# Optimization experiments

Hardware: AMD Instinct MI355X
Metric: run time of the kernel (lower is better)

The kernel has to match this reference:

```python
import jax, jax.numpy as jnp
import numpy as np

V, T, H, N, D, L = 32000, 2048, 4, 4096, 256, 6
K = N // H  # head dim = 1024
EPS = 1e-5


def ln(x):
    # LayerNorm over last dim, no affine (elementwise_affine=False)
    mu = jnp.mean(x, axis=-1, keepdims=True)
    var = jnp.mean(jnp.square(x - mu), axis=-1, keepdims=True)
    return (x - mu) / jnp.sqrt(var + EPS)


def rotate_half(x):
    hd = x.shape[-1]
    return jnp.concatenate([-x[..., hd // 2:], x[..., :hd // 2]], axis=-1)


def rope_tables(seq_len, head_dim):
    inv_freq = 1.0 / (10000.0 ** (jnp.arange(0, head_dim, 2, dtype=jnp.float32) / head_dim))
    t = jnp.arange(seq_len, dtype=jnp.float32)
    freqs = t[:, None] * inv_freq[None, :]          # [T, hd/2]
    emb = jnp.concatenate([freqs, freqs], axis=-1)  # [T, hd]
    return jnp.cos(emb), jnp.sin(emb)


def setup_inputs() -> dict:
    key = jax.random.key(0)
    ks = jax.random.split(key, 7)
    input_ = jax.random.randint(ks[0], (2, T), 0, V, dtype=jnp.int32)
    emb = jax.random.normal(ks[1], (V, D), dtype=jnp.float32) * 0.02
    pos = jax.random.normal(ks[2], (T, D), dtype=jnp.float32) * (1.0 / np.sqrt(L))
    Dx = jax.random.normal(ks[3], (H, D, K), dtype=jnp.float32) * 0.02
    Dy = jax.random.normal(ks[4], (H, D, K), dtype=jnp.float32) * 0.02
    E = jax.random.normal(ks[5], (N, D), dtype=jnp.float32) * 0.02
    readout = jax.random.normal(ks[6], (D, V), dtype=jnp.float32) * 0.02
    return {"input_": input_, "emb": emb, "pos": pos, "Dx": Dx, "Dy": Dy, "E": E, "readout": readout}


def reference(input_, emb, pos, Dx, Dy, E, readout):
    B, Tl = input_.shape
    cos, sin = rope_tables(Tl, K)
    cos = cos[None, None]  # [1,1,T,K]
    sin = sin[None, None]
    v = ln(emb[input_])  # [B,T,D]
    for _ in range(L):
        v = v + pos[None]  # abs pos added every layer
        x = jax.nn.relu(jnp.einsum('btd,hdk->bhtk', v, Dx))  # [B,H,T,K]
        q = x * cos + rotate_half(x) * sin                   # RoPE (Q==K)
        scores = jnp.einsum('bhtk,bhsk->bhts', q, q)         # unnormalized, no softmax
        a = jnp.einsum('bhts,bsd->bhtd', scores, v)          # [B,H,T,D]
        y = jax.nn.relu(jnp.einsum('bhtd,hdk->bhtk', ln(a), Dy)) * x  # gated
        y = y.transpose(0, 2, 1, 3).reshape(B, Tl, H * K)    # [B,T,N]
        v = ln(v + ln(y @ E))
    return v @ readout  # [B,T,V]
```

## Files before the change

kernel.cpp:

```cpp
#include <hip/hip_runtime.h>
#include <hip/hip_bf16.h>

using u16 = unsigned short;

#define BB 2
#define TT 2048
#define DD 256
#define HH_ 4
#define KK 1024
#define NN 4096
#define VV 32000
#define BT 4096
#define LL 6

typedef __attribute__((ext_vector_type(8))) short short8;
typedef __attribute__((ext_vector_type(4))) float f32x4;

__device__ __forceinline__ float b2f(u16 u) {
    union { unsigned int i; float f; } cv; cv.i = ((unsigned int)u) << 16; return cv.f;
}
__device__ __forceinline__ u16 f2b(float f) {
    union { float f; unsigned int i; } cv; cv.f = f;
    const unsigned int u = cv.i;
    return (u16)((u + 0x7fffu + ((u >> 16) & 1u)) >> 16);
}
__device__ __forceinline__ float rdF(const float* p) { return *p; }
__device__ __forceinline__ float rdF(const u16* p)   { return b2f(*p); }
__device__ __forceinline__ void stF(float* p, float v) { *p = v; }
__device__ __forceinline__ void stF(u16* p, float v)   { *p = f2b(v); }

__device__ __forceinline__ float block_sum_256(float val, float* sbuf) {
#pragma unroll
    for (int off = 32; off > 0; off >>= 1)
        val += __shfl_down(val, off, 64);
    const int lane = threadIdx.x & 63;
    const int wid  = threadIdx.x >> 6;
    __syncthreads();
    if (lane == 0) sbuf[wid] = val;
    __syncthreads();
    return sbuf[0] + sbuf[1] + sbuf[2] + sbuf[3];
}

__global__ void k_sincos(float* __restrict__ cosH, float* __restrict__ sinH) {
    const int t = blockIdx.x;
    for (int f = threadIdx.x; f < 512; f += blockDim.x) {
        const double invf = exp(-((double)(2 * f) / (double)KK) * 9.210340371976184);
        const double th = (double)t * invf;
        double s, c;
        sincos(th, &s, &c);
        cosH[t * 512 + f] = (float)c;
        sinH[t * 512 + f] = (float)s;
    }
}

__global__ void k_embed_ln(const int* __restrict__ idx, const float* __restrict__ emb,
                           const float* __restrict__ pos,
                           float* __restrict__ v, u16* __restrict__ vbf) {
    __shared__ float sbuf[4];
    const int r = blockIdx.x;
    const int t = r & (TT - 1);
    const int token = idx[r];
    const float xv = emb[(long)token * DD + threadIdx.x];
    const float mu = block_sum_256(xv, sbuf) * (1.f / DD);
    const float d = xv - mu;
    const float var = block_sum_256(d * d, sbuf) * (1.f / DD);
    const float res = d / sqrtf(var + 1e-5f) + pos[t * DD + threadIdx.x];
    v[(long)r * DD + threadIdx.x] = res;
    vbf[(long)r * DD + threadIdx.x] = f2b(res);
}

__global__ void k_ln_rows_out(const float* __restrict__ a, u16* __restrict__ o) {
    __shared__ float sbuf[4];
    const long r = blockIdx.x;
    const float xv = a[r * DD + threadIdx.x];
    const float mu = block_sum_256(xv, sbuf) * (1.f / DD);
    const float d = xv - mu;
    const float var = block_sum_256(d * d, sbuf) * (1.f / DD);
    o[r * DD + threadIdx.x] = f2b(d / sqrtf(var + 1e-5f));
}

__global__ void k_fin_ln(float* __restrict__ v, const float* __restrict__ zp,
                         const float* __restrict__ pos, u16* __restrict__ vbf,
                         int addp) {
    __shared__ float sbuf[4];
    const long r = blockIdx.x;
    const int t = (int)(r & (TT - 1));
    const long i = r * DD + threadIdx.x;
    const long S = (long)BT * DD;
    const float zv = zp[i] + zp[i + S] + zp[i + 2 * S] + zp[i + 3 * S];
    const float mu1 = block_sum_256(zv, sbuf) * (1.f / DD);
    const float d1 = zv - mu1;
    const float var1 = block_sum_256(d1 * d1, sbuf) * (1.f / DD);
    const float lnz = d1 / sqrtf(var1 + 1e-5f);
    const float u = v[i] + lnz;
    const float mu2 = block_sum_256(u, sbuf) * (1.f / DD);
    const float d2 = u - mu2;
    const float var2 = block_sum_256(d2 * d2, sbuf) * (1.f / DD);
    float res = d2 / sqrtf(var2 + 1e-5f);
    if (addp) res += pos[t * DD + threadIdx.x];
    v[i] = res;
    vbf[i] = f2b(res);
}

template <typename TIN>
__global__ __launch_bounds__(256)
void k_trans(const TIN* __restrict__ in, u16* __restrict__ out, int R, int C) {
    __shared__ float tile[32][33];
    const long zo = (long)blockIdx.z * (long)R * (long)C;
    const int r0 = blockIdx.y * 32, c0 = blockIdx.x * 32;
    const int tx = threadIdx.x & 31, ty = threadIdx.x >> 5;
#pragma unroll
    for (int u = 0; u < 32; u += 8)
        tile[ty + u][tx] = rdF(&in[zo + (long)(r0 + ty + u) * C + c0 + tx]);
    __syncthreads();
#pragma unroll
    for (int u = 0; u < 32; u += 8)
        out[zo + (long)(c0 + ty + u) * R + r0 + tx] = f2b(tile[tx][ty + u]);
}

__global__ __launch_bounds__(256)
void k_rope_t(const u16* __restrict__ x, const float* __restrict__ cosH,
              const float* __restrict__ sinH, u16* __restrict__ q, u16* __restrict__ qT) {
    __shared__ u16 Sa[64][72];
    __shared__ u16 Sb[64][72];
    const long zoff = (long)blockIdx.z * TT * KK;
    const int t0 = blockIdx.y * 64;
    const int klo = blockIdx.x * 64;
    const int khi = klo + 512;
    const int tx = threadIdx.x & 63;
    const int ty = threadIdx.x >> 6;
#pragma unroll
    for (int u = 0; u < 64; u += 4) {
        const int t = t0 + u + ty;
        const long rb = (long)t * KK;
        const float xa = b2f(x[zoff + rb + klo + tx]);
        const float xb = b2f(x[zoff + rb + khi + tx]);
        const float ca = cosH[t * 512 + klo + tx];
        const float sa = sinH[t * 512 + klo + tx];
        const float qa = xa * ca - xb * sa;
        const float qb = xb * ca + xa * sa;
        const u16 qab = f2b(qa), qbb = f2b(qb);
        q[zoff + rb + klo + tx] = qab;
        q[zoff + rb + khi + tx] = qbb;
        Sa[u + ty][tx] = qab;
        Sb[u + ty][tx] = qbb;
    }
    __syncthreads();
#pragma unroll
    for (int u = 0; u < 64; u += 4) {
        const int r = u + ty;
        qT[zoff + (long)(klo + r) * TT + t0 + tx] = Sa[tx][r];
        qT[zoff + (long)(khi + r) * TT + t0 + tx] = Sb[tx][r];
    }
}

template <int EPI, typename TC>
__global__ __launch_bounds__(256)
void gemm_mfma(const u16* __restrict__ Ab, const u16* __restrict__ Btb,
               TC* __restrict__ Cb, const u16* __restrict__ Gb,
               int M, int N, int Kin, int lda, int ldb, int ldc, int ldg,
               long sAo, long sAi, long sBo, long sBi,
               long sCo, long sCi, long sGo, long sGi, int HH)
{
    const int z = blockIdx.z;
    const int zo = z / HH, zi = z - zo * HH;
    const u16* A  = Ab  + zo * sAo + zi * sAi;
    const u16* Bt = Btb + zo * sBo + zi * sBi;
    TC* C = Cb + zo * sCo + zi * sCi;
    const u16* G = (EPI == 2) ? (Gb + zo * sGo + zi * sGi) : nullptr;

    const int m0 = blockIdx.y * 128;
    const int n0 = blockIdx.x * 128;
    const int tid = threadIdx.x;
    const int lane = tid & 63;
    const int wv = tid >> 6;
    const int wr = (wv >> 1) * 64;
    const int wc = (wv & 1) * 64;

    __shared__ u16 As[128 * 64];
    __shared__ u16 Bs[128 * 64];

    f32x4 acc[4][4];
    const f32x4 vzero = {0.f, 0.f, 0.f, 0.f};
#pragma unroll
    for (int i = 0; i < 4; ++i)
#pragma unroll
        for (int j = 0; j < 4; ++j) acc[i][j] = vzero;

    const int rbase = tid >> 3;
    const int slot  = tid & 7;
    const u16* Abase = A  + (long)(m0 + rbase) * lda + slot * 8;
    const u16* Bbase = Bt + (long)(n0 + rbase) * ldb + slot * 8;
    const int ldsU = (tid & 192) * 8;

    const int rl = lane & 15;
    const int kg = lane >> 4;

    for (int k0 = 0; k0 < Kin; k0 += 64) {
#pragma unroll
        for (int it = 0; it < 4; ++it) {
            __builtin_amdgcn_global_load_lds(
                (const __attribute__((address_space(1))) unsigned int*)(Abase + (long)it * 32 * lda + k0),
                (__attribute__((address_space(3))) unsigned int*)(As + it * 2048 + ldsU),
                16, 0, 0);
            __builtin_amdgcn_global_load_lds(
                (const __attribute__((address_space(1))) unsigned int*)(Bbase + (long)it * 32 * ldb + k0),
                (__attribute__((address_space(3))) unsigned int*)(Bs + it * 2048 + ldsU),
                16, 0, 0);
        }
        __syncthreads();
#pragma unroll
        for (int kk = 0; kk < 2; ++kk) {
            const int sl = kk * 4 + kg;
            short8 af[4], bfr[4];
#pragma unroll
            for (int i = 0; i < 4; ++i)
                af[i] = *(const short8*)(&As[(wr + i * 16 + rl) * 64 + sl * 8]);
#pragma unroll
            for (int j = 0; j < 4; ++j)
                bfr[j] = *(const short8*)(&Bs[(wc + j * 16 + rl) * 64 + sl * 8]);
#pragma unroll
            for (int i = 0; i < 4; ++i)
#pragma unroll
                for (int j = 0; j < 4; ++j)
                    acc[i][j] = __builtin_amdgcn_mfma_f32_16x16x32_bf16(af[i], bfr[j], acc[i][j], 0, 0, 0);
        }
        __syncthreads();
    }

#pragma unroll
    for (int i = 0; i < 4; ++i) {
#pragma unroll
        for (int rr = 0; rr < 4; ++rr) {
            const int m = m0 + wr + i * 16 + kg * 4 + rr;
#pragma unroll
            for (int j = 0; j < 4; ++j) {
                const int n = n0 + wc + j * 16 + rl;
                float val = acc[i][j][rr];
                if (EPI >= 1) val = fmaxf(val, 0.f);
                if (EPI == 2) val *= b2f(G[(long)m * ldg + n]);
                stF(&C[(long)m * ldc + n], val);
            }
        }
    }
}

extern "C" void kernel_launch(void* const* d_in, const int* in_sizes, int n_in,
                              void* d_out, int out_size, void* d_ws, size_t ws_size,
                              hipStream_t stream)
{
    const int* input_ = (const int*)d_in[0];
    const float* emb = (const float*)d_in[1];
    const float* pos = (const float*)d_in[2];
    const float* Dx = (const float*)d_in[3];
    const float* Dy = (const float*)d_in[4];
    const float* E  = (const float*)d_in[5];
    const float* readout = (const float*)d_in[6];
    float* out = (float*)d_out;

    char* base = (char*)d_ws;
    const long MiB = 1024 * 1024;
    float* v     = (float*)(base + 0);
    float* zpart = (float*)(base + 4  * MiB);
    float* cosH  = (float*)(base + 20 * MiB);
    float* sinH  = (float*)(base + 24 * MiB);
    u16* vbf  = (u16*)(base + 28 * MiB);
    u16* vbfT = (u16*)(base + 30 * MiB);
    u16* wT   = (u16*)(base + 32 * MiB);
    u16* x    = (u16*)(base + 36 * MiB);
    u16* q    = (u16*)(base + 68 * MiB);
    u16* y    = q;
    u16* qT   = (u16*)(base + 100 * MiB);
    float* a  = (float*)qT;
    u16* lnab = (u16*)(base + 132 * MiB);
    u16* DxT  = (u16*)(base + 140 * MiB);
    u16* DyT  = (u16*)(base + 142 * MiB);
    u16* ET   = (u16*)(base + 144 * MiB);
    u16* roT  = (u16*)(base + 146 * MiB);

    k_trans<float><<<dim3(KK / 32, DD / 32, HH_), 256, 0, stream>>>(Dx, DxT, DD, KK);
    k_trans<float><<<dim3(KK / 32, DD / 32, HH_), 256, 0, stream>>>(Dy, DyT, DD, KK);
    k_trans<float><<<dim3(DD / 32, NN / 32, 1),   256, 0, stream>>>(E, ET, NN, DD);
    k_trans<float><<<dim3(VV / 32, DD / 32, 1),   256, 0, stream>>>(readout, roT, DD, VV);
    k_sincos<<<TT, 256, 0, stream>>>(cosH, sinH);
    k_embed_ln<<<BT, 256, 0, stream>>>(input_, emb, pos, v, vbf);

    for (int l = 0; l < LL; ++l) {
        k_trans<u16><<<dim3(DD / 32, TT / 32, BB), 256, 0, stream>>>(vbf, vbfT, TT, DD);

        gemm_mfma<1, u16><<<dim3(KK / 128, TT / 128, BB * HH_), 256, 0, stream>>>(
            vbf, DxT, x, nullptr,
            TT, KK, DD, DD, DD, KK, 0,
            (long)TT * DD, 0, 0, (long)KK * DD,
            (long)HH_ * TT * KK, (long)TT * KK, 0, 0, HH_);

        k_rope_t<<<dim3(8, TT / 64, BB * HH_), 256, 0, stream>>>(x, cosH, sinH, q, qT);

        gemm_mfma<0, u16><<<dim3(KK / 128, DD / 128, BB * HH_), 256, 0, stream>>>(
            vbfT, qT, wT, nullptr,
            DD, KK, TT, TT, TT, KK, 0,
            (long)DD * TT, 0, (long)HH_ * KK * TT, (long)KK * TT,
            (long)HH_ * DD * KK, (long)DD * KK, 0, 0, HH_);

        gemm_mfma<0, float><<<dim3(DD / 128, TT / 128, BB * HH_), 256, 0, stream>>>(
            q, wT, a, nullptr,
            TT, DD, KK, KK, KK, DD, 0,
            (long)HH_ * TT * KK, (long)TT * KK, (long)HH_ * DD * KK, (long)DD * KK,
            (long)HH_ * TT * DD, (long)TT * DD, 0, 0, HH_);

        k_ln_rows_out<<<BB * HH_ * TT, 256, 0, stream>>>(a, lnab);

        gemm_mfma<2, u16><<<dim3(KK / 128, TT / 128, BB * HH_), 256, 0, stream>>>(
            lnab, DyT, y, x,
            TT, KK, DD, DD, DD, NN, KK,
            (long)HH_ * TT * DD, (long)TT * DD, 0, (long)KK * DD,
            (long)TT * NN, (long)KK, (long)HH_ * TT * KK, (long)TT * KK, HH_);

        gemm_mfma<0, float><<<dim3(DD / 128, BT / 128, 4), 256, 0, stream>>>(
            y, ET, zpart, nullptr,
            BT, DD, KK, NN, NN, DD, 0,
            1024, 0, 1024, 0,
            (long)BT * DD, 0, 0, 0, 1);

        k_fin_ln<<<BT, 256, 0, stream>>>(v, zpart, pos, vbf, (l < LL - 1) ? 1 : 0);
    }

    gemm_mfma<0, float><<<dim3(VV / 128, BT / 128, 1), 256, 0, stream>>>(
        vbf, roT, out, nullptr,
        BT, VV, DD, DD, DD, VV, 0,
        0, 0, 0, 0, 0, 0, 0, 0, 1);
}
```

Baseline: 1.746 ms.

## Add split-K partial GEMMs with reductions and 256-row tiles for wide GEMMs

Generalizes the MFMA GEMM with a split-K dimension (ZB, per-split strides) and a templated M tile (BM=256 with 512 threads). The q^T v GEMM is split 4 ways into fp32 partials reduced by a new kernel. The a GEMM is split 2 ways, with the reduction folded into the LayerNorm. The y@E GEMM is split 8 ways instead of 4. The goal is more blocks for the small-output, long-K GEMMs, which otherwise underfill the GPU. The cost is extra fp32 partial traffic, a larger workspace, and more reduction work. The larger tiles for the x, y and readout GEMMs aim to improve reuse.

```diff
diff --git a/kernel.cpp b/kernel.cpp
--- a/kernel.cpp
+++ b/kernel.cpp
@@ -14,6 +14,7 @@
 #define LL 6
 
 typedef __attribute__((ext_vector_type(8))) short short8;
+typedef __attribute__((ext_vector_type(4))) short short4v;
 typedef __attribute__((ext_vector_type(4))) float f32x4;
 
 __device__ __forceinline__ float b2f(u16 u) {
@@ -72,11 +73,13 @@
 __global__ void k_ln_rows_out(const float* __restrict__ a, u16* __restrict__ o) {
     __shared__ float sbuf[4];
     const long r = blockIdx.x;
-    const float xv = a[r * DD + threadIdx.x];
+    const long S = (long)BB * HH_ * TT * DD;
+    const long i = r * DD + threadIdx.x;
+    const float xv = a[i] + a[i + S];
     const float mu = block_sum_256(xv, sbuf) * (1.f / DD);
     const float d = xv - mu;
     const float var = block_sum_256(d * d, sbuf) * (1.f / DD);
-    o[r * DD + threadIdx.x] = f2b(d / sqrtf(var + 1e-5f));
+    o[i] = f2b(d / sqrtf(var + 1e-5f));
 }
 
 __global__ void k_fin_ln(float* __restrict__ v, const float* __restrict__ zp,
@@ -87,7 +90,9 @@
     const int t = (int)(r & (TT - 1));
     const long i = r * DD + threadIdx.x;
     const long S = (long)BT * DD;
-    const float zv = zp[i] + zp[i + S] + zp[i + 2 * S] + zp[i + 3 * S];
+    float zv = 0.f;
+#pragma unroll
+    for (int s = 0; s < 8; ++s) zv += zp[i + s * S];
     const float mu1 = block_sum_256(zv, sbuf) * (1.f / DD);
     const float d1 = zv - mu1;
     const float var1 = block_sum_256(d1 * d1, sbuf) * (1.f / DD);
@@ -100,6 +105,19 @@
     if (addp) res += pos[t * DD + threadIdx.x];
     v[i] = res;
     vbf[i] = f2b(res);
+}
+
+__global__ void k_red_wT(const float* __restrict__ wp, u16* __restrict__ o) {
+    const long S = (long)BB * HH_ * DD * KK;
+    const long i0 = ((long)blockIdx.x * 256 + threadIdx.x) * 4;
+    f32x4 a = *(const f32x4*)(wp + i0);
+    f32x4 b = *(const f32x4*)(wp + i0 + S);
+    f32x4 c = *(const f32x4*)(wp + i0 + 2 * S);
+    f32x4 d = *(const f32x4*)(wp + i0 + 3 * S);
+    short4v r;
+#pragma unroll
+    for (int j = 0; j < 4; ++j) r[j] = (short)f2b(a[j] + b[j] + c[j] + d[j]);
+    *(short4v*)(o + i0) = r;
 }
 
 template <typename TIN>
@@ -154,22 +172,27 @@
     }
 }
 
-template <int EPI, typename TC>
-__global__ __launch_bounds__(256)
+template <int BM, int EPI, typename TC>
+__global__ __launch_bounds__(BM * 2)
 void gemm_mfma(const u16* __restrict__ Ab, const u16* __restrict__ Btb,
                TC* __restrict__ Cb, const u16* __restrict__ Gb,
                int M, int N, int Kin, int lda, int ldb, int ldc, int ldg,
                long sAo, long sAi, long sBo, long sBi,
-               long sCo, long sCi, long sGo, long sGi, int HH)
+               long sCo, long sCi, long sGo, long sGi,
+               int HH, int ZB, long sAk, long sBk, long sCk)
 {
-    const int z = blockIdx.z;
+    constexpr int THREADS = BM * 2;
+    constexpr int RPI = THREADS / 8;
+    constexpr int B_ITS = 1024 / THREADS;
+    int z = blockIdx.z;
+    const int s = z / ZB; z -= s * ZB;
     const int zo = z / HH, zi = z - zo * HH;
-    const u16* A  = Ab  + zo * sAo + zi * sAi;
-    const u16* Bt = Btb + zo * sBo + zi * sBi;
-    TC* C = Cb + zo * sCo + zi * sCi;
+    const u16* A  = Ab  + zo * sAo + zi * sAi + (long)s * sAk;
+    const u16* Bt = Btb + zo * sBo + zi * sBi + (long)s * sBk;
+    TC* C = Cb + zo * sCo + zi * sCi + (long)s * sCk;
     const u16* G = (EPI == 2) ? (Gb + zo * sGo + zi * sGi) : nullptr;
 
-    const int m0 = blockIdx.y * 128;
+    const int m0 = blockIdx.y * BM;
     const int n0 = blockIdx.x * 128;
     const int tid = threadIdx.x;
     const int lane = tid & 63;
@@ -177,7 +200,7 @@
     const int wr = (wv >> 1) * 64;
     const int wc = (wv & 1) * 64;
 
-    __shared__ u16 As[128 * 64];
+    __shared__ u16 As[BM * 64];
     __shared__ u16 Bs[128 * 64];
 
     f32x4 acc[4][4];
@@ -191,7 +214,7 @@
     const int slot  = tid & 7;
     const u16* Abase = A  + (long)(m0 + rbase) * lda + slot * 8;
     const u16* Bbase = Bt + (long)(n0 + rbase) * ldb + slot * 8;
-    const int ldsU = (tid & 192) * 8;
+    const int wub = (tid & ~63) * 8;
 
     const int rl = lane & 15;
     const int kg = lane >> 4;
@@ -200,12 +223,15 @@
 #pragma unroll
         for (int it = 0; it < 4; ++it) {
             __builtin_amdgcn_global_load_lds(
-                (const __attribute__((address_space(1))) unsigned int*)(Abase + (long)it * 32 * lda + k0),
-                (__attribute__((address_space(3))) unsigned int*)(As + it * 2048 + ldsU),
+                (const __attribute__((address_space(1))) unsigned int*)(Abase + (long)it * RPI * lda + k0),
+                (__attribute__((address_space(3))) unsigned int*)(As + it * (THREADS * 8) + wub),
                 16, 0, 0);
+        }
+#pragma unroll
+        for (int it = 0; it < B_ITS; ++it) {
             __builtin_amdgcn_global_load_lds(
-                (const __attribute__((address_space(1))) unsigned int*)(Bbase + (long)it * 32 * ldb + k0),
-                (__attribute__((address_space(3))) unsigned int*)(Bs + it * 2048 + ldsU),
+                (const __attribute__((address_space(1))) unsigned int*)(Bbase + (long)it * RPI * ldb + k0),
+                (__attribute__((address_space(3))) unsigned int*)(Bs + it * (THREADS * 8) + wub),
                 16, 0, 0);
         }
         __syncthreads();
@@ -262,21 +288,22 @@
     const long MiB = 1024 * 1024;
     float* v     = (float*)(base + 0);
     float* zpart = (float*)(base + 4  * MiB);
-    float* cosH  = (float*)(base + 20 * MiB);
-    float* sinH  = (float*)(base + 24 * MiB);
-    u16* vbf  = (u16*)(base + 28 * MiB);
-    u16* vbfT = (u16*)(base + 30 * MiB);
-    u16* wT   = (u16*)(base + 32 * MiB);
-    u16* x    = (u16*)(base + 36 * MiB);
-    u16* q    = (u16*)(base + 68 * MiB);
-    u16* y    = q;
-    u16* qT   = (u16*)(base + 100 * MiB);
-    float* a  = (float*)qT;
-    u16* lnab = (u16*)(base + 132 * MiB);
-    u16* DxT  = (u16*)(base + 140 * MiB);
-    u16* DyT  = (u16*)(base + 142 * MiB);
-    u16* ET   = (u16*)(base + 144 * MiB);
-    u16* roT  = (u16*)(base + 146 * MiB);
+    float* cosH  = (float*)(base + 36 * MiB);
+    float* sinH  = (float*)(base + 40 * MiB);
+    u16* vbf   = (u16*)(base + 44 * MiB);
+    u16* vbfT  = (u16*)(base + 46 * MiB);
+    u16* wTb   = (u16*)(base + 48 * MiB);
+    float* wpart = (float*)(base + 52 * MiB);
+    float* apart = wpart;
+    u16* x     = (u16*)(base + 84 * MiB);
+    u16* q     = (u16*)(base + 116 * MiB);
+    u16* y     = q;
+    u16* qT    = (u16*)(base + 148 * MiB);
+    u16* lnab  = (u16*)(base + 180 * MiB);
+    u16* DxT   = (u16*)(base + 188 * MiB);
+    u16* DyT   = (u16*)(base + 190 * MiB);
+    u16* ET    = (u16*)(base + 192 * MiB);
+    u16* roT   = (u16*)(base + 194 * MiB);
 
     k_trans<float><<<dim3(KK / 32, DD / 32, HH_), 256, 0, stream>>>(Dx, DxT, DD, KK);
     k_trans<float><<<dim3(KK / 32, DD / 32, HH_), 256, 0, stream>>>(Dy, DyT, DD, KK);
@@ -288,45 +315,52 @@
     for (int l = 0; l < LL; ++l) {
         k_trans<u16><<<dim3(DD / 32, TT / 32, BB), 256, 0, stream>>>(vbf, vbfT, TT, DD);
 
-        gemm_mfma<1, u16><<<dim3(KK / 128, TT / 128, BB * HH_), 256, 0, stream>>>(
+        gemm_mfma<256, 1, u16><<<dim3(KK / 128, TT / 256, BB * HH_), 512, 0, stream>>>(
             vbf, DxT, x, nullptr,
             TT, KK, DD, DD, DD, KK, 0,
             (long)TT * DD, 0, 0, (long)KK * DD,
-            (long)HH_ * TT * KK, (long)TT * KK, 0, 0, HH_);
+            (long)HH_ * TT * KK, (long)TT * KK, 0, 0,
+            HH_, BB * HH_, 0, 0, 0);
 
         k_rope_t<<<dim3(8, TT / 64, BB * HH_), 256, 0, stream>>>(x, cosH, sinH, q, qT);
 
-        gemm_mfma<0, u16><<<dim3(KK / 128, DD / 128, BB * HH_), 256, 0, stream>>>(
-            vbfT, qT, wT, nullptr,
-            DD, KK, TT, TT, TT, KK, 0,
+        gemm_mfma<128, 0, float><<<dim3(KK / 128, DD / 128, 4 * BB * HH_), 256, 0, stream>>>(
+            vbfT, qT, wpart, nullptr,
+            DD, KK, TT / 4, TT, TT, KK, 0,
             (long)DD * TT, 0, (long)HH_ * KK * TT, (long)KK * TT,
-            (long)HH_ * DD * KK, (long)DD * KK, 0, 0, HH_);
-
-        gemm_mfma<0, float><<<dim3(DD / 128, TT / 128, BB * HH_), 256, 0, stream>>>(
-            q, wT, a, nullptr,
-            TT, DD, KK, KK, KK, DD, 0,
+            (long)HH_ * DD * KK, (long)DD * KK, 0, 0,
+            HH_, BB * HH_, 512, 512, (long)BB * HH_ * DD * KK);
+
+        k_red_wT<<<2048, 256, 0, stream>>>(wpart, wTb);
+
+        gemm_mfma<128, 0, float><<<dim3(DD / 128, TT / 128, 2 * BB * HH_), 256, 0, stream>>>(
+            q, wTb, apart, nullptr,
+            TT, DD, KK / 2, KK, KK, DD, 0,
             (long)HH_ * TT * KK, (long)TT * KK, (long)HH_ * DD * KK, (long)DD * KK,
-            (long)HH_ * TT * DD, (long)TT * DD, 0, 0, HH_);
-
-        k_ln_rows_out<<<BB * HH_ * TT, 256, 0, stream>>>(a, lnab);
-
-        gemm_mfma<2, u16><<<dim3(KK / 128, TT / 128, BB * HH_), 256, 0, stream>>>(
+            (long)HH_ * TT * DD, (long)TT * DD, 0, 0,
+            HH_, BB * HH_, 512, 512, (long)BB * HH_ * TT * DD);
+
+        k_ln_rows_out<<<BB * HH_ * TT, 256, 0, stream>>>(apart, lnab);
+
+        gemm_mfma<256, 2, u16><<<dim3(KK / 128, TT / 256, BB * HH_), 512, 0, stream>>>(
             lnab, DyT, y, x,
             TT, KK, DD, DD, DD, NN, KK,
             (long)HH_ * TT * DD, (long)TT * DD, 0, (long)KK * DD,
-            (long)TT * NN, (long)KK, (long)HH_ * TT * KK, (long)TT * KK, HH_);
-
-        gemm_mfma<0, float><<<dim3(DD / 128, BT / 128, 4), 256, 0, stream>>>(
+            (long)TT * NN, (long)KK, (long)HH_ * TT * KK, (long)TT * KK,
+            HH_, BB * HH_, 0, 0, 0);
+
+        gemm_mfma<128, 0, float><<<dim3(DD / 128, BT / 128, 8), 256, 0, stream>>>(
             y, ET, zpart, nullptr,
-            BT, DD, KK, NN, NN, DD, 0,
-            1024, 0, 1024, 0,
-            (long)BT * DD, 0, 0, 0, 1);
+            BT, DD, NN / 8, NN, NN, DD, 0,
+            0, 0, 0, 0, 0, 0, 0, 0,
+            1, 1, 512, 512, (long)BT * DD);
 
         k_fin_ln<<<BT, 256, 0, stream>>>(v, zpart, pos, vbf, (l < LL - 1) ? 1 : 0);
     }
 
-    gemm_mfma<0, float><<<dim3(VV / 128, BT / 128, 1), 256, 0, stream>>>(
+    gemm_mfma<256, 0, float><<<dim3(VV / 128, BT / 256, 1), 512, 0, stream>>>(
         vbf, roT, out, nullptr,
         BT, VV, DD, DD, DD, VV, 0,
-        0, 0, 0, 0, 0, 0, 0, 0, 1);
-}
+        0, 0, 0, 0, 0, 0, 0, 0,
+        1, 1, 0, 0, 0);
+}
```

New measurement: 1.551 ms. -11.2%, faster.
